# Kernel optimization log

Hardware: AMD Instinct MI355X
Metric: run time of the kernel (lower is better)

## Reference

```python
import jax, jax.numpy as jnp
import numpy as np

D_MODEL, D_K, D_V, HEADS = 512, 8, 8, 6
EPS = 1e-5


def setup_inputs() -> dict:
    key = jax.random.key(0)
    ks = jax.random.split(key, 16)
    B, S = 16, 1024
    inp = {
        'q_input': jax.random.normal(ks[0], (B, S, D_MODEL), jnp.float32),
        'k_input': jax.random.normal(ks[1], (B, S, D_MODEL), jnp.float32),
        'v_input': jax.random.normal(ks[2], (B, S, D_MODEL), jnp.float32),
        'mask': jax.random.randint(ks[3], (B, S, S), 0, 2).astype(bool),
        'Wq': jax.random.normal(ks[4], (D_MODEL, D_K * HEADS), jnp.float32) * 0.04,
        'bq': jax.random.normal(ks[5], (D_K * HEADS,), jnp.float32) * 0.02,
        'Wk': jax.random.normal(ks[6], (D_MODEL, D_K * HEADS), jnp.float32) * 0.04,
        'bk': jax.random.normal(ks[7], (D_K * HEADS,), jnp.float32) * 0.02,
        'Wv': jax.random.normal(ks[8], (D_MODEL, D_V * HEADS), jnp.float32) * 0.04,
        'bv': jax.random.normal(ks[9], (D_V * HEADS,), jnp.float32) * 0.02,
        'Wo': jax.random.normal(ks[10], (HEADS * D_K, D_MODEL), jnp.float32) * 0.1,
        'bo': jax.random.normal(ks[11], (D_MODEL,), jnp.float32) * 0.02,
        'ln_w': 1.0 + jax.random.normal(ks[12], (D_MODEL,), jnp.float32) * 0.02,
        'ln_b': jax.random.normal(ks[13], (D_MODEL,), jnp.float32) * 0.02,
    }
    return inp


def reference(q_input, k_input, v_input, mask, Wq, bq, Wk, bk, Wv, bv, Wo, bo, ln_w, ln_b):
    B, S, _ = q_input.shape
    # projections -> [B, H, S, d]
    q_s = (q_input @ Wq + bq).reshape(B, S, HEADS, D_K).transpose(0, 2, 1, 3)
    k_s = (k_input @ Wk + bk).reshape(B, S, HEADS, D_K).transpose(0, 2, 1, 3)
    v_s = (v_input @ Wv + bv).reshape(B, S, HEADS, D_V).transpose(0, 2, 1, 3)
    # scaled dot-product with masked_fill(mask, 1e-9) as in the original (fills VALUE, not -inf)
    scores = jnp.einsum('bhqd,bhkd->bhqk', q_s, k_s) / np.sqrt(D_K).astype(np.float32)
    scores = jnp.where(mask[:, None, :, :], jnp.float32(1e-9), scores)
    attn = jax.nn.softmax(scores, axis=-1)
    out = jnp.einsum('bhqk,bhkd->bhqd', attn, v_s)  # [B,H,S,d_v]
    out = out.transpose(0, 2, 1, 3).reshape(B, S, HEADS * D_K)
    out = out @ Wo + bo
    x = q_input + out  # residual
    mu = jnp.mean(x, axis=-1, keepdims=True)
    var = jnp.var(x, axis=-1, keepdims=True)
    return (x - mu) * jax.lax.rsqrt(var + EPS) * ln_w + ln_b
```

## Files before the change

### kernel.cpp

```cpp
#include <hip/hip_runtime.h>

constexpr int B = 16;
constexpr int S = 1024;
constexpr int DM = 512;
constexpr int H = 6;
constexpr int DK = 8;
constexpr int NJ = H * DK;
constexpr int BS = B * S;
constexpr int WB_ELEMS = 16 * NJ * 32;

typedef __attribute__((ext_vector_type(8))) short bf16x8;
typedef __attribute__((ext_vector_type(8))) _Float16 half8;
typedef __attribute__((ext_vector_type(4))) _Float16 half4;
typedef __attribute__((ext_vector_type(4))) float floatx4;

#define LOG2E 1.4426950408889634f
#define QSCALE (0.35355339059327373f * LOG2E)

__device__ inline ushort f2bf(float f) {
  unsigned int u = __builtin_bit_cast(unsigned int, f);
  return (ushort)((u + 0x7FFFu + ((u >> 16) & 1u)) >> 16);
}

__global__ __launch_bounds__(256) void maskbits_kernel(
    const int* __restrict__ mask, unsigned long long* __restrict__ bits) {
  int wave = threadIdx.x >> 6, lane = threadIdx.x & 63;
  int row = blockIdx.x * 4 + wave;
  const int* mrow = mask + (size_t)row * S;
  unsigned long long* brow = bits + (size_t)row * 16;
  int koff = ((lane >> 5) << 5) + 2 * (lane & 15) + ((lane >> 4) & 1);
#pragma unroll
  for (int c = 0; c < 16; c++) {
    int v = mrow[c * 64 + koff];
    unsigned long long bal = __ballot(v != 0);
    if (lane == 0) brow[c] = bal;
  }
}

__global__ __launch_bounds__(256) void wprep_kernel(
    const float* __restrict__ Wq, const float* __restrict__ Wk,
    const float* __restrict__ Wv, ushort* __restrict__ Wb,
    uint2* __restrict__ VBf) {
  int m = blockIdx.x;
  if (m < 3) {
    const float* W = (m == 0) ? Wq : (m == 1) ? Wk : Wv;
    ushort* dst = Wb + (size_t)m * WB_ELEMS;
    for (int e = threadIdx.x; e < WB_ELEMS; e += 256) {
      int kc = e / 1536;
      int rem = e - kc * 1536;
      int n = rem >> 5, kj = rem & 31;
      dst[e] = f2bf(W[(size_t)(kc * 32 + kj) * NJ + n]);
    }
  } else {
    int bh = m - 3;
    for (int i = threadIdx.x; i < 2048; i += 256) {
      int tile = i >> 5;
      int li = i & 31;
      int g = li >> 3, dd = 8 + (li & 7);
      uint hv = (dd == 8) ? 0x3C003C00u : 0u;
      uint2 val; val.x = hv; val.y = hv;
      VBf[((size_t)bh * 64 + tile) * 64 + g * 16 + dd] = val;
    }
  }
}

__global__ __launch_bounds__(128) void proj_kernel(
    const float* __restrict__ q_in, const float* __restrict__ k_in,
    const float* __restrict__ v_in, const ushort* __restrict__ Wb,
    const float* __restrict__ bq, const float* __restrict__ bk,
    const float* __restrict__ bv,
    ushort* __restrict__ Qo, ushort* __restrict__ Ko, ushort* __restrict__ Vo) {
  int m = blockIdx.y;
  const float* x    = (m == 0) ? q_in : (m == 1) ? k_in : v_in;
  const float* bias = (m == 0) ? bq   : (m == 1) ? bk   : bv;
  ushort* out       = (m == 0) ? Qo   : (m == 1) ? Ko   : Vo;
  float oscale      = (m == 0) ? QSCALE : 1.0f;
  const ushort* Wg  = Wb + (size_t)m * WB_ELEMS;

  __shared__ ushort Xl[32 * DM];

  int t = threadIdx.x;
  int r0 = blockIdx.x * 32;
  int wave = t >> 6, lane = t & 63;
  int n16 = lane & 15, quad = lane >> 4;

  {
    const float4* xs = (const float4*)(x + (size_t)r0 * DM);
    char* xb = (char*)Xl;
#pragma unroll 8
    for (int i = 0; i < 32; i++) {
      int f4 = t + (i << 7);
      float4 v = xs[f4];
      int r = f4 >> 7;
      int c = (f4 & 127) << 2;
      ushort4 hv;
      hv.x = f2bf(v.x); hv.y = f2bf(v.y);
      hv.z = f2bf(v.z); hv.w = f2bf(v.w);
      int off = ((r << 10) | (c << 1)) ^ ((r & 7) << 4);
      *(ushort4*)(xb + off) = hv;
    }
  }

  floatx4 acc0 = {0.f, 0.f, 0.f, 0.f};
  floatx4 acc1 = {0.f, 0.f, 0.f, 0.f};
  floatx4 acc2 = {0.f, 0.f, 0.f, 0.f};

  __syncthreads();

  int rr = wave * 16 + n16;
  const char* xrd = (const char*)Xl;
#pragma unroll
  for (int kc = 0; kc < 16; kc++) {
    int off = ((rr << 10) | (kc << 6) | (quad << 4)) ^ ((n16 & 7) << 4);
    bf16x8 a = *(const bf16x8*)(xrd + off);
    const ushort* wbase = Wg + (kc * 48 + n16) * 32 + quad * 8;
    bf16x8 b0 = *(const bf16x8*)(wbase);
    bf16x8 b1 = *(const bf16x8*)(wbase + 16 * 32);
    bf16x8 b2 = *(const bf16x8*)(wbase + 32 * 32);
    acc0 = __builtin_amdgcn_mfma_f32_16x16x32_bf16(a, b0, acc0, 0, 0, 0);
    acc1 = __builtin_amdgcn_mfma_f32_16x16x32_bf16(a, b1, acc1, 0, 0, 0);
    acc2 = __builtin_amdgcn_mfma_f32_16x16x32_bf16(a, b2, acc2, 0, 0, 0);
  }

  int baseR = r0 + wave * 16 + quad * 4;
#pragma unroll
  for (int j = 0; j < 3; j++) {
    floatx4 a = (j == 0) ? acc0 : (j == 1) ? acc1 : acc2;
    int n = j * 16 + n16;
    float bn = bias[n];
    int h = n >> 3, d = n & 7;
#pragma unroll
    for (int r = 0; r < 4; r++) {
      int R = baseR + r;
      int b = R >> 10, s = R & 1023;
      float fv = (a[r] + bn) * oscale;
      if (m == 2) {
        size_t idx =
            ((((size_t)(b * H + h) * 64 + (s >> 4)) * 64) +
             ((s >> 2) & 3) * 16 + d) * 4 + (s & 3);
        out[idx] = __builtin_bit_cast(ushort, (_Float16)fv);
      } else {
        out[(((size_t)(b * H + h)) * S + s) * 8 + d] = f2bf(fv);
      }
    }
  }
}

__global__ __launch_bounds__(256, 3) void attn_kernel(
    const ushort* __restrict__ Qg, const ushort* __restrict__ Kg,
    const ushort* __restrict__ VBg ,
    const uint* __restrict__ bits32, float* __restrict__ A) {
  int bh = blockIdx.x >> 4;
  int qt = blockIdx.x & 15;
  int b = bh / H, h = bh % H;
  int q0 = qt * 64;

  __shared__ uint4 Kl[1024];
  __shared__ uint2 Vl[64 * 64];

  int t = threadIdx.x;
  int wave = t >> 6, lane = t & 63;
  int quad = lane >> 4, n16 = lane & 15;

  {
    const uint4* Ksrc = (const uint4*)(Kg + (size_t)bh * S * 8);
#pragma unroll
    for (int i = 0; i < 4; i++) Kl[t + i * 256] = Ksrc[t + i * 256];
    const uint2* Vsrc = (const uint2*)VBg + (size_t)bh * (64 * 64);
#pragma unroll
    for (int i = 0; i < 16; i++) Vl[t + i * 256] = Vsrc[t + i * 256];
  }

  bf16x8 aq = {0, 0, 0, 0, 0, 0, 0, 0};
  if (quad == 0)
    aq = *(const bf16x8*)&Qg[((size_t)bh * S + q0 + wave * 16 + n16) * 8];

  const uint* mrow = bits32 + (size_t)(b * S + q0 + wave * 16 + n16) * 32;

  __syncthreads();

  floatx4 acc0 = {0.f, 0.f, 0.f, 0.f};
  floatx4 acc1 = {0.f, 0.f, 0.f, 0.f};
  const floatx4 zero = {0.f, 0.f, 0.f, 0.f};
  int sh0 = 2 * quad;

  const ushort* kb = (const ushort*)Kl + n16 * 8;
  const uint2* vbb = Vl + lane;

#pragma unroll
  for (int cc = 0; cc < 8; cc++) {
    uint4 mq = *(const uint4*)(mrow + cc * 4);
#pragma unroll
    for (int ci = 0; ci < 4; ci++) {
      int c = cc * 4 + ci;
      uint mw = (ci == 0) ? mq.x : (ci == 1) ? mq.y : (ci == 2) ? mq.z : mq.w;

      bf16x8 ak0 = *(const bf16x8*)(kb + c * 256);
      bf16x8 ak1 = *(const bf16x8*)(kb + c * 256 + 128);
      uint2 vb0 = vbb[(2 * c) * 64];
      uint2 vb1 = vbb[(2 * c + 1) * 64];

      floatx4 s0 = __builtin_amdgcn_mfma_f32_16x16x32_bf16(ak0, aq, zero, 0, 0, 0);
      floatx4 s1 = __builtin_amdgcn_mfma_f32_16x16x32_bf16(ak1, aq, zero, 0, 0, 0);

      float p0 = exp2f(fminf(s0[0], 15.f)), p1 = exp2f(fminf(s0[1], 15.f));
      float p2 = exp2f(fminf(s0[2], 15.f)), p3 = exp2f(fminf(s0[3], 15.f));
      float p4 = exp2f(fminf(s1[0], 15.f)), p5 = exp2f(fminf(s1[1], 15.f));
      float p6 = exp2f(fminf(s1[2], 15.f)), p7 = exp2f(fminf(s1[3], 15.f));
      uint w0 = __builtin_bit_cast(uint, __builtin_amdgcn_cvt_pkrtz(p0, p1));
      uint w1 = __builtin_bit_cast(uint, __builtin_amdgcn_cvt_pkrtz(p2, p3));
      uint w2 = __builtin_bit_cast(uint, __builtin_amdgcn_cvt_pkrtz(p4, p5));
      uint w3 = __builtin_bit_cast(uint, __builtin_amdgcn_cvt_pkrtz(p6, p7));

      uint m0 = ((mw >> sh0) & 0x10001u) * 0xFFFFu;
      uint m1 = ((mw >> (sh0 + 1)) & 0x10001u) * 0xFFFFu;
      uint m2 = ((mw >> (sh0 + 8)) & 0x10001u) * 0xFFFFu;
      uint m3 = ((mw >> (sh0 + 9)) & 0x10001u) * 0xFFFFu;
      w0 = (m0 & 0x3C003C00u) | (~m0 & w0);
      w1 = (m1 & 0x3C003C00u) | (~m1 & w1);
      w2 = (m2 & 0x3C003C00u) | (~m2 & w2);
      w3 = (m3 & 0x3C003C00u) | (~m3 & w3);

      uint2 pu0; pu0.x = w0; pu0.y = w1;
      uint2 pu1; pu1.x = w2; pu1.y = w3;
      half4 pa0 = __builtin_bit_cast(half4, pu0);
      half4 pa1 = __builtin_bit_cast(half4, pu1);

      acc0 = __builtin_amdgcn_mfma_f32_16x16x16f16(
          pa0, __builtin_bit_cast(half4, vb0), acc0, 0, 0, 0);
      acc1 = __builtin_amdgcn_mfma_f32_16x16x16f16(
          pa1, __builtin_bit_cast(half4, vb1), acc1, 0, 0, 0);
    }
  }

#pragma unroll
  for (int r = 0; r < 4; r++) {
    float sum = acc0[r] + acc1[r];
    float dnm = __shfl(sum, (lane & 48) | 8, 64);
    if (n16 < 8) {
      int qg = q0 + wave * 16 + quad * 4 + r;
      A[((size_t)(b * S + qg)) * NJ + h * 8 + n16] = sum / dnm;
    }
  }
}

__global__ __launch_bounds__(256) void out_ln_kernel(
    const float* __restrict__ A, const float* __restrict__ Wo,
    const float* __restrict__ bo, const float* __restrict__ qin,
    const float* __restrict__ lnw, const float* __restrict__ lnb,
    float* __restrict__ out) {
  int r0 = blockIdx.x * 8;
  int t = threadIdx.x;
  __shared__ float As[8 * NJ];
#pragma unroll
  for (int i = t; i < 8 * NJ; i += 256) As[i] = A[(size_t)r0 * NJ + i];
  __syncthreads();

  int c0 = t, c1 = t + 256;
  float acc0[8], acc1[8];
#pragma unroll
  for (int r = 0; r < 8; r++) { acc0[r] = 0.f; acc1[r] = 0.f; }

#pragma unroll 4
  for (int j = 0; j < NJ; j++) {
    float w0 = Wo[(size_t)j * DM + c0];
    float w1 = Wo[(size_t)j * DM + c1];
#pragma unroll
    for (int r = 0; r < 8; r++) {
      float a = As[r * NJ + j];
      acc0[r] += a * w0;
      acc1[r] += a * w1;
    }
  }

  float b0 = bo[c0], b1 = bo[c1];
  float y0[8], y1[8], ssum[8], sq[8];
#pragma unroll
  for (int r = 0; r < 8; r++) {
    y0[r] = acc0[r] + b0 + qin[(size_t)(r0 + r) * DM + c0];
    y1[r] = acc1[r] + b1 + qin[(size_t)(r0 + r) * DM + c1];
    ssum[r] = y0[r] + y1[r];
    sq[r] = y0[r] * y0[r] + y1[r] * y1[r];
  }

  int wave = t >> 6, lane = t & 63;
  __shared__ float reds[4][8], redq[4][8];
#pragma unroll
  for (int r = 0; r < 8; r++) {
    float s = ssum[r], qq = sq[r];
#pragma unroll
    for (int off = 32; off > 0; off >>= 1) {
      s += __shfl_xor(s, off, 64);
      qq += __shfl_xor(qq, off, 64);
    }
    if (lane == 0) { reds[wave][r] = s; redq[wave][r] = qq; }
  }
  __syncthreads();

  float lw0 = lnw[c0], lw1 = lnw[c1], lb0 = lnb[c0], lb1 = lnb[c1];
#pragma unroll
  for (int r = 0; r < 8; r++) {
    float s = (reds[0][r] + reds[1][r]) + (reds[2][r] + reds[3][r]);
    float qq = (redq[0][r] + redq[1][r]) + (redq[2][r] + redq[3][r]);
    float mu = s * (1.f / 512.f);
    float var = qq * (1.f / 512.f) - mu * mu;
    float rstd = rsqrtf(var + 1e-5f);
    out[(size_t)(r0 + r) * DM + c0] = (y0[r] - mu) * rstd * lw0 + lb0;
    out[(size_t)(r0 + r) * DM + c1] = (y1[r] - mu) * rstd * lw1 + lb1;
  }
}

extern "C" void kernel_launch(void* const* d_in, const int* in_sizes, int n_in,
                              void* d_out, int out_size, void* d_ws,
                              size_t ws_size, hipStream_t stream) {
  const float* q_in = (const float*)d_in[0];
  const float* k_in = (const float*)d_in[1];
  const float* v_in = (const float*)d_in[2];
  const int* mask = (const int*)d_in[3];
  const float* Wq = (const float*)d_in[4];
  const float* bq = (const float*)d_in[5];
  const float* Wk = (const float*)d_in[6];
  const float* bk = (const float*)d_in[7];
  const float* Wv = (const float*)d_in[8];
  const float* bv = (const float*)d_in[9];
  const float* Wo = (const float*)d_in[10];
  const float* bo = (const float*)d_in[11];
  const float* lnw = (const float*)d_in[12];
  const float* lnb = (const float*)d_in[13];
  float* out = (float*)d_out;

  constexpr size_t QKV = (size_t)B * H * S * DK;
  ushort* base = (ushort*)d_ws;
  ushort* Qw = base;
  ushort* Kw = base + QKV;
  ushort* VBw = base + 2 * QKV;
  float* Aw = (float*)(base + 4 * QKV);
  unsigned long long* bits = (unsigned long long*)(Aw + (size_t)BS * NJ);
  ushort* Wb = (ushort*)(bits + (size_t)BS * 16);

  maskbits_kernel<<<BS / 4, 256, 0, stream>>>(mask, bits);
  wprep_kernel<<<3 + B * H, 256, 0, stream>>>(Wq, Wk, Wv, Wb, (uint2*)VBw);
  proj_kernel<<<dim3(BS / 32, 3), 128, 0, stream>>>(
      q_in, k_in, v_in, Wb, bq, bk, bv, Qw, Kw, VBw);
  attn_kernel<<<(B * H * S) / 64, 256, 0, stream>>>(
      Qw, Kw, VBw, (const uint*)bits, Aw);
  out_ln_kernel<<<BS / 8, 256, 0, stream>>>(Aw, Wo, bo, q_in, lnw, lnb, out);
}
```

Measured before the change: 317.9 us.

## Read K/V directly from global memory in attention kernel, drop LDS staging

The attention kernel no longer stages each head's K and V (48KB) into shared memory behind a barrier. Each wave now loads K and V fragments straight from global memory, relying on L2/L1 caching. Launch bounds rise to 6 blocks per CU, block IDs are swizzled so blocks sharing a head spread across XCDs, and the chunk loop unroll drops to 2. The aim is higher occupancy and no LDS fill or sync cost, at the price of repeated global/cache reads of K and V by every block and wave.

```diff
diff --git a/kernel.cpp b/kernel.cpp
--- a/kernel.cpp
+++ b/kernel.cpp
@@ -146,48 +146,36 @@
   }
 }
 
-__global__ __launch_bounds__(256, 3) void attn_kernel(
+__global__ __launch_bounds__(256, 6) void attn_kernel(
     const ushort* __restrict__ Qg, const ushort* __restrict__ Kg,
     const ushort* __restrict__ VBg ,
     const uint* __restrict__ bits32, float* __restrict__ A) {
-  int bh = blockIdx.x >> 4;
-  int qt = blockIdx.x & 15;
+  int bid = blockIdx.x;
+  int swz = (bid & 7) * 192 + (bid >> 3);
+  int bh = swz >> 4;
+  int qt = swz & 15;
   int b = bh / H, h = bh % H;
   int q0 = qt * 64;
-
-  __shared__ uint4 Kl[1024];
-  __shared__ uint2 Vl[64 * 64];
 
   int t = threadIdx.x;
   int wave = t >> 6, lane = t & 63;
   int quad = lane >> 4, n16 = lane & 15;
 
-  {
-    const uint4* Ksrc = (const uint4*)(Kg + (size_t)bh * S * 8);
-#pragma unroll
-    for (int i = 0; i < 4; i++) Kl[t + i * 256] = Ksrc[t + i * 256];
-    const uint2* Vsrc = (const uint2*)VBg + (size_t)bh * (64 * 64);
-#pragma unroll
-    for (int i = 0; i < 16; i++) Vl[t + i * 256] = Vsrc[t + i * 256];
-  }
+  const ushort* Kbase = Kg + (size_t)bh * S * 8;
+  const uint2* VB = (const uint2*)VBg + (size_t)bh * (64 * 64);
 
   bf16x8 aq = {0, 0, 0, 0, 0, 0, 0, 0};
   if (quad == 0)
     aq = *(const bf16x8*)&Qg[((size_t)bh * S + q0 + wave * 16 + n16) * 8];
 
   const uint* mrow = bits32 + (size_t)(b * S + q0 + wave * 16 + n16) * 32;
-
-  __syncthreads();
 
   floatx4 acc0 = {0.f, 0.f, 0.f, 0.f};
   floatx4 acc1 = {0.f, 0.f, 0.f, 0.f};
   const floatx4 zero = {0.f, 0.f, 0.f, 0.f};
   int sh0 = 2 * quad;
 
-  const ushort* kb = (const ushort*)Kl + n16 * 8;
-  const uint2* vbb = Vl + lane;
-
-#pragma unroll
+#pragma unroll 2
   for (int cc = 0; cc < 8; cc++) {
     uint4 mq = *(const uint4*)(mrow + cc * 4);
 #pragma unroll
@@ -195,10 +183,10 @@
       int c = cc * 4 + ci;
       uint mw = (ci == 0) ? mq.x : (ci == 1) ? mq.y : (ci == 2) ? mq.z : mq.w;
 
-      bf16x8 ak0 = *(const bf16x8*)(kb + c * 256);
-      bf16x8 ak1 = *(const bf16x8*)(kb + c * 256 + 128);
-      uint2 vb0 = vbb[(2 * c) * 64];
-      uint2 vb1 = vbb[(2 * c + 1) * 64];
+      bf16x8 ak0 = *(const bf16x8*)&Kbase[(size_t)(c * 32 + n16) * 8];
+      bf16x8 ak1 = *(const bf16x8*)&Kbase[(size_t)(c * 32 + 16 + n16) * 8];
+      uint2 vb0 = VB[(2 * c) * 64 + lane];
+      uint2 vb1 = VB[(2 * c + 1) * 64 + lane];
 
       floatx4 s0 = __builtin_amdgcn_mfma_f32_16x16x32_bf16(ak0, aq, zero, 0, 0, 0);
       floatx4 s1 = __builtin_amdgcn_mfma_f32_16x16x32_bf16(ak1, aq, zero, 0, 0, 0);
```

After: 316.2 us. No clear change (-0.5%).
